# Performance work log

Measured on AMD Instinct MI355X. Metric: run time of the kernel, lower is better.

The kernel has to match this reference:

```python
import jax, jax.numpy as jnp
import numpy as np

DIM = 1024
HEADS = 16
HIDDEN = 2048  # dim * mlp_ratio
EPS = 1e-6


def _rmsnorm(x, scale):
    # faithful to torch: x * (scale / (norm / (sqrt(d) + eps)))
    norm = jnp.linalg.norm(x, axis=-1, keepdims=True)
    return x * (scale * (x.shape[-1] ** 0.5 + EPS) / norm)


def setup_inputs() -> dict:
    key = jax.random.key(0)
    ks = jax.random.split(key, 8)
    B, N, C = 4, 4096, DIM
    s = 0.02
    return {
        "x": jax.random.normal(ks[0], (B, N, C), dtype=jnp.float32),
        "scale1": jnp.ones((C,), jnp.float32),
        "scale2": jnp.ones((C,), jnp.float32),
        "gamma": jnp.ones((C,), jnp.float32),
        "qkv_w": jax.random.normal(ks[1], (3 * C, C), jnp.float32) * s,
        "proj_w": jax.random.normal(ks[2], (C, C), jnp.float32) * s,
        "proj_b": jnp.zeros((C,), jnp.float32),
        "conv1_w": jax.random.normal(ks[3], (HIDDEN, C), jnp.float32) * s,
        "conv1_b": jnp.zeros((HIDDEN,), jnp.float32),
        "conv2_w": jax.random.normal(ks[4], (C, HIDDEN), jnp.float32) * s,
        "conv2_b": jnp.zeros((C,), jnp.float32),
    }


def reference(x, scale1, scale2, gamma, qkv_w, proj_w, proj_b,
              conv1_w, conv1_b, conv2_w, conv2_b):
    B, N, C = x.shape
    h, d = HEADS, C // HEADS

    # ---- attention branch ----
    xn = _rmsnorm(x, scale1)
    qkv = jnp.einsum('bnc,fc->bnf', xn, qkv_w)           # [B,N,3C]
    qkv = qkv.reshape(B, N, 3, h, d).transpose(2, 0, 3, 1, 4)  # [3,B,h,N,d]
    q, k, v = qkv[0], qkv[1], qkv[2]
    phi = lambda t: jnp.exp(-0.5 * t * t)
    q, k = phi(q), phi(k)
    kv = jnp.einsum('bhnd,bhne->bhde', k, v)             # [B,h,d,d]
    z = 1.0 / (jnp.einsum('bhnd,bhd->bhn', q, k.sum(2)) + 1e-6)
    out = jnp.einsum('bhnd,bhde,bhn->bhne', q, kv, z)    # [B,h,N,d]
    out = out.transpose(0, 2, 1, 3).reshape(B, N, C)
    attn = jnp.einsum('bnc,oc->bno', out, proj_w) + proj_b
    x = x + gamma * attn

    # ---- MLP branch (1x1 convs == per-token linear) ----
    xn2 = _rmsnorm(x, scale2)
    hdd = jax.nn.gelu(jnp.einsum('bnc,hc->bnh', xn2, conv1_w) + conv1_b, approximate=False)
    mlp = jnp.einsum('bnh,ch->bnc', hdd, conv2_w) + conv2_b
    return x + gamma * mlp
```

## Files before the change

kernel.cpp:

```cpp
#include <hip/hip_runtime.h>
#include <hip/hip_bf16.h>
#include <math.h>

#define MTOK 16384

typedef __attribute__((ext_vector_type(8))) short bf16x8;
typedef __attribute__((ext_vector_type(4))) float f32x4;

__device__ __forceinline__ float bf2f(ushort u) {
  union { unsigned int u; float f; } c; c.u = ((unsigned int)u) << 16; return c.f;
}
__device__ __forceinline__ ushort f2bf(float f) {
  union { float f; unsigned int u; } c; c.f = f;
  unsigned int r = c.u + 0x7fffu + ((c.u >> 16) & 1u);
  return (ushort)(r >> 16);
}

__device__ __forceinline__ void gload_lds16(const void* g, void* l) {
  __builtin_amdgcn_global_load_lds(
      (const __attribute__((address_space(1))) unsigned int*)g,
      (__attribute__((address_space(3))) unsigned int*)l, 16, 0, 0);
}

__global__ __launch_bounds__(256)
void f32_to_bf16_k(const float* __restrict__ in, ushort* __restrict__ out, int n4) {
  int i = blockIdx.x * 256 + threadIdx.x;
  if (i >= n4) return;
  float4 v = *(const float4*)&in[(size_t)i * 4];
  ushort4 o;
  o.x = f2bf(v.x); o.y = f2bf(v.y); o.z = f2bf(v.z); o.w = f2bf(v.w);
  *(ushort4*)&out[(size_t)i * 4] = o;
}

__global__ __launch_bounds__(256)
void f32_to_bf16_rs_k(const float* __restrict__ in, ushort* __restrict__ out,
                      int n4, const float* __restrict__ rs, int K_in) {
  int i = blockIdx.x * 256 + threadIdx.x;
  if (i >= n4) return;
  float g = rs[(i * 4) / K_in];
  float4 v = *(const float4*)&in[(size_t)i * 4];
  ushort4 o;
  o.x = f2bf(v.x * g); o.y = f2bf(v.y * g); o.z = f2bf(v.z * g); o.w = f2bf(v.w * g);
  *(ushort4*)&out[(size_t)i * 4] = o;
}

__global__ __launch_bounds__(256)
void gbias_k(const float* __restrict__ gamma, const float* __restrict__ bias,
             float* __restrict__ gb, int n) {
  int i = blockIdx.x * 256 + threadIdx.x;
  if (i < n) gb[i] = gamma[i] * bias[i];
}

__global__ __launch_bounds__(256)
void rmsnorm_k(const float* __restrict__ x, const float* __restrict__ scale,
               ushort* __restrict__ out) {
  __shared__ float red[4];
  int row = blockIdx.x;
  int t = threadIdx.x;
  const float* xr = x + (size_t)row * 1024;
  float4 v = *(const float4*)&xr[t * 4];
  float s = v.x*v.x + v.y*v.y + v.z*v.z + v.w*v.w;
  #pragma unroll
  for (int off = 32; off > 0; off >>= 1) s += __shfl_xor(s, off);
  if ((t & 63) == 0) red[t >> 6] = s;
  __syncthreads();
  float tot = red[0] + red[1] + red[2] + red[3];
  float rn = (32.0f + 1e-6f) / sqrtf(tot);
  float4 sc = *(const float4*)&scale[t * 4];
  ushort4 o;
  o.x = f2bf(v.x * rn * sc.x);
  o.y = f2bf(v.y * rn * sc.y);
  o.z = f2bf(v.z * rn * sc.z);
  o.w = f2bf(v.w * rn * sc.w);
  *(ushort4*)&out[(size_t)row * 1024 + t * 4] = o;
}

template<int EPI>
__global__ __launch_bounds__(256, 2)
void gemm_bt(const ushort* __restrict__ A, const ushort* __restrict__ W,
             void* __restrict__ outp, const float* __restrict__ bias,
             const float* __restrict__ resid,
             ushort* __restrict__ kTp, ushort* __restrict__ vTp,
             int M, int F, int K) {
  __shared__ ushort lA[2][128 * 32];
  __shared__ ushort lB[2][128 * 32];
  const int tid = threadIdx.x;
  const int lane = tid & 63;
  const int w = tid >> 6;
  const int nBn = F >> 7;
  const int cpx = (int)gridDim.x >> 3;
  const int tile = ((int)blockIdx.x & 7) * cpx + ((int)blockIdx.x >> 3);
  const int bm = tile / nBn;
  const int bn = tile % nBn;
  const int brow = bm << 7, bcol = bn << 7;
  const int wr = w >> 1, wc = w & 1;

  const int srow = (w << 4) + (lane >> 2);
  const int key = (srow >> 1) & 3;
  const int kcsrc = (lane & 3) ^ key;
  const ushort* gA0 = A + (size_t)(brow + srow) * K + kcsrc * 8;
  const ushort* gA1 = gA0 + (size_t)64 * K;
  const ushort* gB0 = W + (size_t)(bcol + srow) * K + kcsrc * 8;
  const ushort* gB1 = gB0 + (size_t)64 * K;

  auto stage = [&](int bf, int k0) {
    gload_lds16(gA0 + k0, &lA[bf][w * 512]);
    gload_lds16(gA1 + k0, &lA[bf][2048 + w * 512]);
    gload_lds16(gB0 + k0, &lB[bf][w * 512]);
    gload_lds16(gB1 + k0, &lB[bf][2048 + w * 512]);
  };

  const int frow = lane & 15;
  const int kq = lane >> 4;

  f32x4 acc[4][4];
  #pragma unroll
  for (int i = 0; i < 4; ++i)
    #pragma unroll
    for (int j = 0; j < 4; ++j) acc[i][j] = (f32x4){0.f, 0.f, 0.f, 0.f};

  stage(0, 0);
  __syncthreads();

  int buf = 0;
  for (int k0 = 0; k0 < K; k0 += 32, buf ^= 1) {
    if (k0 + 32 < K) stage(buf ^ 1, k0 + 32);

    bf16x8 af[4], bfr[4];
    #pragma unroll
    for (int mi = 0; mi < 4; ++mi) {
      int row = (wr << 6) + (mi << 4) + frow;
      int off = (row << 5) + ((kq ^ ((row >> 1) & 3)) << 3);
      af[mi] = *(const bf16x8*)&lA[buf][off];
    }
    #pragma unroll
    for (int ni = 0; ni < 4; ++ni) {
      int row = (wc << 6) + (ni << 4) + frow;
      int off = (row << 5) + ((kq ^ ((row >> 1) & 3)) << 3);
      bfr[ni] = *(const bf16x8*)&lB[buf][off];
    }
    #pragma unroll
    for (int mi = 0; mi < 4; ++mi)
      #pragma unroll
      for (int ni = 0; ni < 4; ++ni)
        acc[mi][ni] = __builtin_amdgcn_mfma_f32_16x16x32_bf16(
            af[mi], bfr[ni], acc[mi][ni], 0, 0, 0);
    __syncthreads();
  }

  #pragma unroll
  for (int mi = 0; mi < 4; ++mi) {
    #pragma unroll
    for (int ni = 0; ni < 4; ++ni) {
      int col = bcol + (wc << 6) + (ni << 4) + frow;
      int rbase = brow + (wr << 6) + (mi << 4) + (kq << 2);
      if (EPI == 0) {
        if (col < 1024) {
          #pragma unroll
          for (int r = 0; r < 4; ++r) {
            float v = acc[mi][ni][r];
            ((ushort*)outp)[(size_t)(rbase + r) * 1024 + col] =
                f2bf(__expf(-0.5f * v * v));
          }
        } else {
          bool isk = col < 2048;
          int c = col - (isk ? 1024 : 2048);
          int b = rbase >> 12, n = rbase & 4095;
          ushort4 o;
          #pragma unroll
          for (int r = 0; r < 4; ++r) {
            float v = acc[mi][ni][r];
            if (isk) v = __expf(-0.5f * v * v);
            ((ushort*)&o)[r] = f2bf(v);
          }
          ushort* dst = (isk ? kTp : vTp) +
                        ((size_t)(b * 16 + (c >> 6)) * 64 + (c & 63)) * 4096 + n;
          *(ushort4*)dst = o;
        }
      } else {
        #pragma unroll
        for (int r = 0; r < 4; ++r) {
          int row = rbase + r;
          float v = acc[mi][ni][r];
          size_t idx = (size_t)row * F + col;
          if (EPI == 1) {
            ((float*)outp)[idx] = resid[idx] + v + bias[col];
          } else {
            float t2 = v + bias[col];
            float y = 0.79788456f * (t2 + 0.044715f * t2 * t2 * t2);
            float e = __expf(2.0f * y);
            float th = (e - 1.0f) / (e + 1.0f);
            ((ushort*)outp)[idx] = f2bf(0.5f * t2 * (1.0f + th));
          }
        }
      }
    }
  }
}

__global__ __launch_bounds__(256)
void attn_kv_mfma(const ushort* __restrict__ kT, const ushort* __restrict__ vT,
                  float* __restrict__ kvT, float* __restrict__ ksum) {
  __shared__ float red[4][4096];
  int bi = blockIdx.x;
  int ksl = bi & 7, h = (bi >> 3) & 15, b = bi >> 7;
  int tid = threadIdx.x, lane = tid & 63, w = tid >> 6;
  int frow = lane & 15, kq = lane >> 4;
  const size_t bh = (size_t)(b * 16 + h) * 64;
  const ushort* vb = vT + bh * 4096;
  const ushort* kb = kT + bh * 4096;
  int tk0 = ksl * 512 + w * 128;

  f32x4 acc[4][4];
  #pragma unroll
  for (int i = 0; i < 4; ++i)
    #pragma unroll
    for (int j = 0; j < 4; ++j) acc[i][j] = (f32x4){0.f, 0.f, 0.f, 0.f};
  float kpart[4] = {0.f, 0.f, 0.f, 0.f};

  #pragma unroll
  for (int kstep = 0; kstep < 4; ++kstep) {
    int tok = tk0 + kstep * 32 + kq * 8;
    bf16x8 af[4], bfr[4];
    #pragma unroll
    for (int mi = 0; mi < 4; ++mi)
      af[mi] = *(const bf16x8*)&vb[(size_t)(mi * 16 + frow) * 4096 + tok];
    #pragma unroll
    for (int ni = 0; ni < 4; ++ni) {
      bfr[ni] = *(const bf16x8*)&kb[(size_t)(ni * 16 + frow) * 4096 + tok];
      #pragma unroll
      for (int j = 0; j < 8; ++j) kpart[ni] += bf2f((ushort)bfr[ni][j]);
    }
    #pragma unroll
    for (int mi = 0; mi < 4; ++mi)
      #pragma unroll
      for (int ni = 0; ni < 4; ++ni)
        acc[mi][ni] = __builtin_amdgcn_mfma_f32_16x16x32_bf16(
            af[mi], bfr[ni], acc[mi][ni], 0, 0, 0);
  }

  #pragma unroll
  for (int ni = 0; ni < 4; ++ni) {
    kpart[ni] += __shfl_xor(kpart[ni], 16);
    kpart[ni] += __shfl_xor(kpart[ni], 32);
  }
  if (lane < 16) {
    #pragma unroll
    for (int ni = 0; ni < 4; ++ni)
      atomicAdd(&ksum[(b * 16 + h) * 64 + ni * 16 + frow], kpart[ni]);
  }

  #pragma unroll
  for (int mi = 0; mi < 4; ++mi)
    #pragma unroll
    for (int ni = 0; ni < 4; ++ni)
      #pragma unroll
      for (int r = 0; r < 4; ++r)
        red[w][(mi * 16 + kq * 4 + r) * 64 + ni * 16 + frow] = acc[mi][ni][r];
  __syncthreads();
  float* kvg = kvT + (size_t)(b * 16 + h) * 4096;
  for (int i = tid; i < 4096; i += 256) {
    float s = red[0][i] + red[1][i] + red[2][i] + red[3][i];
    atomicAdd(&kvg[i], s);
  }
}

__global__ __launch_bounds__(256)
void attn_out_mfma(const ushort* __restrict__ qb, const float* __restrict__ kvT,
                   const float* __restrict__ ksum, ushort* __restrict__ ao) {
  __shared__ ushort skv[64 * 72];
  __shared__ float sks[64];
  int bi = blockIdx.x;
  int c = bi & 15, h = (bi >> 4) & 15, b = bi >> 8;
  int tid = threadIdx.x, lane = tid & 63, w = tid >> 6;
  int frow = lane & 15, kq = lane >> 4;
  const float* kvg = kvT + (size_t)(b * 16 + h) * 4096;
  for (int i = tid; i < 4096; i += 256)
    skv[(i >> 6) * 72 + (i & 63)] = f2bf(kvg[i]);
  if (tid < 64) sks[tid] = ksum[(b * 16 + h) * 64 + tid];
  __syncthreads();

  int m0 = b * 4096 + c * 256 + w * 64;
  f32x4 acc[4][4];
  #pragma unroll
  for (int i = 0; i < 4; ++i)
    #pragma unroll
    for (int j = 0; j < 4; ++j) acc[i][j] = (f32x4){0.f, 0.f, 0.f, 0.f};
  float dp[4] = {0.f, 0.f, 0.f, 0.f};

  #pragma unroll
  for (int kst = 0; kst < 2; ++kst) {
    int d0 = kst * 32 + kq * 8;
    bf16x8 af[4], bfr[4];
    #pragma unroll
    for (int mi = 0; mi < 4; ++mi)
      af[mi] = *(const bf16x8*)&qb[(size_t)(m0 + mi * 16 + frow) * 1024 + h * 64 + d0];
    #pragma unroll
    for (int ni = 0; ni < 4; ++ni)
      bfr[ni] = *(const bf16x8*)&skv[(ni * 16 + frow) * 72 + d0];
    #pragma unroll
    for (int mi = 0; mi < 4; ++mi) {
      float s = 0.f;
      #pragma unroll
      for (int j = 0; j < 8; ++j) s += bf2f((ushort)af[mi][j]) * sks[d0 + j];
      dp[mi] += s;
    }
    #pragma unroll
    for (int mi = 0; mi < 4; ++mi)
      #pragma unroll
      for (int ni = 0; ni < 4; ++ni)
        acc[mi][ni] = __builtin_amdgcn_mfma_f32_16x16x32_bf16(
            af[mi], bfr[ni], acc[mi][ni], 0, 0, 0);
  }

  #pragma unroll
  for (int mi = 0; mi < 4; ++mi) {
    dp[mi] += __shfl_xor(dp[mi], 16);
    dp[mi] += __shfl_xor(dp[mi], 32);
  }

  #pragma unroll
  for (int mi = 0; mi < 4; ++mi)
    #pragma unroll
    for (int ni = 0; ni < 4; ++ni)
      #pragma unroll
      for (int r = 0; r < 4; ++r) {
        float dotv = __shfl(dp[mi], (kq << 2) + r);
        float z = 1.f / (dotv + 1e-6f);
        int mrow = m0 + mi * 16 + kq * 4 + r;
        ao[(size_t)mrow * 1024 + h * 64 + ni * 16 + frow] =
            f2bf(acc[mi][ni][r] * z);
      }
}

extern "C" void kernel_launch(void* const* d_in, const int* in_sizes, int n_in,
                              void* d_out, int out_size, void* d_ws, size_t ws_size,
                              hipStream_t stream) {
  const float* x       = (const float*)d_in[0];
  const float* scale1  = (const float*)d_in[1];
  const float* scale2  = (const float*)d_in[2];
  const float* gamma   = (const float*)d_in[3];
  const float* qkv_w   = (const float*)d_in[4];
  const float* proj_w  = (const float*)d_in[5];
  const float* proj_b  = (const float*)d_in[6];
  const float* conv1_w = (const float*)d_in[7];
  const float* conv1_b = (const float*)d_in[8];
  const float* conv2_w = (const float*)d_in[9];
  const float* conv2_b = (const float*)d_in[10];
  float* out = (float*)d_out;

  char* ws = (char*)d_ws;
  size_t off = 0;
  auto alloc = [&](size_t bytes) {
    void* p = ws + off;
    off += (bytes + 255) & ~(size_t)255;
    return p;
  };
  ushort* xn     = (ushort*)alloc((size_t)MTOK * 1024 * 2);
  ushort* qb     = (ushort*)alloc((size_t)MTOK * 1024 * 2);
  ushort* kT     = (ushort*)alloc((size_t)MTOK * 1024 * 2);
  ushort* vT     = (ushort*)alloc((size_t)MTOK * 1024 * 2);
  ushort* attn_o = (ushort*)alloc((size_t)MTOK * 1024 * 2);
  float*  kvT    = (float*)alloc((size_t)(4 * 16 * 64 * 64 + 4 * 16 * 64) * 4);
  float*  ksum   = kvT + 4 * 16 * 64 * 64;
  ushort* wq = (ushort*)alloc((size_t)3072 * 1024 * 2);
  ushort* wp = (ushort*)alloc((size_t)1024 * 1024 * 2);
  ushort* w1 = (ushort*)alloc((size_t)2048 * 1024 * 2);
  ushort* w2 = (ushort*)alloc((size_t)1024 * 2048 * 2);
  float*  gbp = (float*)alloc(1024 * 4);
  float*  gbc = (float*)alloc(1024 * 4);
  ushort* hid = kT;
  if (off > ws_size) return;

  hipMemsetAsync(kvT, 0, (size_t)(4 * 16 * 64 * 64 + 4 * 16 * 64) * 4, stream);
  f32_to_bf16_k<<<3072, 256, 0, stream>>>(qkv_w, wq, 786432);
  f32_to_bf16_rs_k<<<1024, 256, 0, stream>>>(proj_w, wp, 262144, gamma, 1024);
  f32_to_bf16_k<<<2048, 256, 0, stream>>>(conv1_w, w1, 524288);
  f32_to_bf16_rs_k<<<2048, 256, 0, stream>>>(conv2_w, w2, 524288, gamma, 2048);
  gbias_k<<<4, 256, 0, stream>>>(gamma, proj_b, gbp, 1024);
  gbias_k<<<4, 256, 0, stream>>>(gamma, conv2_b, gbc, 1024);

  rmsnorm_k<<<MTOK, 256, 0, stream>>>(x, scale1, xn);
  gemm_bt<0><<<128 * 24, 256, 0, stream>>>(xn, wq, qb, nullptr, nullptr,
                                           kT, vT, MTOK, 3072, 1024);
  attn_kv_mfma<<<512, 256, 0, stream>>>(kT, vT, kvT, ksum);
  attn_out_mfma<<<1024, 256, 0, stream>>>(qb, kvT, ksum, attn_o);
  gemm_bt<1><<<128 * 8, 256, 0, stream>>>(attn_o, wp, out, gbp, x,
                                          nullptr, nullptr, MTOK, 1024, 1024);

  rmsnorm_k<<<MTOK, 256, 0, stream>>>(out, scale2, xn);
  gemm_bt<2><<<128 * 16, 256, 0, stream>>>(xn, w1, hid, conv1_b, nullptr,
                                           nullptr, nullptr, MTOK, 2048, 1024);
  gemm_bt<1><<<128 * 8, 256, 0, stream>>>(hid, w2, out, gbc, out,
                                          nullptr, nullptr, MTOK, 1024, 2048);
}
```

Baseline: 463.4 us.

## Switch GEMM to 32x32 MFMA and fuse second RMSNorm into proj epilogue

The GEMM inner loop now uses 32x32x16 bf16 MFMA with 2x2 fragments per wave instead of 4x4 16x16x32 fragments, and every epilogue is rewritten for the new accumulator layout. The proj GEMM gets a new epilogue that writes the residual output, emits unnormalized scale2-weighted bf16 activations, and accumulates per-row sum of squares through LDS and global atomics. A small kernel turns those sums into reciprocal norms, which the conv1 GEMM epilogue applies per row. This removes the separate rmsnorm pass over the fp32 residual, at the cost of atomics, heavier epilogue traffic, and a bf16 rounding of the pre-normalized value.

After: 524.6 us. 1.13x slower.

```diff
diff --git a/kernel.cpp b/kernel.cpp
--- a/kernel.cpp
+++ b/kernel.cpp
@@ -6,6 +6,7 @@
 
 typedef __attribute__((ext_vector_type(8))) short bf16x8;
 typedef __attribute__((ext_vector_type(4))) float f32x4;
+typedef __attribute__((ext_vector_type(16))) float f32x16;
 
 __device__ __forceinline__ float bf2f(ushort u) {
   union { unsigned int u; float f; } c; c.u = ((unsigned int)u) << 16; return c.f;
@@ -49,6 +50,12 @@
              float* __restrict__ gb, int n) {
   int i = blockIdx.x * 256 + threadIdx.x;
   if (i < n) gb[i] = gamma[i] * bias[i];
+}
+
+__global__ __launch_bounds__(256)
+void rn_k(const float* __restrict__ sumsq, float* __restrict__ rn, int n) {
+  int i = blockIdx.x * 256 + threadIdx.x;
+  if (i < n) rn[i] = (32.0f + 1e-6f) / sqrtf(sumsq[i]);
 }
 
 __global__ __launch_bounds__(256)
@@ -81,6 +88,8 @@
              void* __restrict__ outp, const float* __restrict__ bias,
              const float* __restrict__ resid,
              ushort* __restrict__ kTp, ushort* __restrict__ vTp,
+             const float* __restrict__ escale, const float* __restrict__ rowscale,
+             float* __restrict__ sumsq, ushort* __restrict__ xnout,
              int M, int F, int K) {
   __shared__ ushort lA[2][128 * 32];
   __shared__ ushort lB[2][128 * 32];
@@ -110,14 +119,16 @@
     gload_lds16(gB1 + k0, &lB[bf][2048 + w * 512]);
   };
 
-  const int frow = lane & 15;
-  const int kq = lane >> 4;
-
-  f32x4 acc[4][4];
-  #pragma unroll
-  for (int i = 0; i < 4; ++i)
-    #pragma unroll
-    for (int j = 0; j < 4; ++j) acc[i][j] = (f32x4){0.f, 0.f, 0.f, 0.f};
+  const int l31 = lane & 31;
+  const int lh = lane >> 5;
+
+  f32x16 acc16[2][2];
+  #pragma unroll
+  for (int i = 0; i < 2; ++i)
+    #pragma unroll
+    for (int j = 0; j < 2; ++j)
+      #pragma unroll
+      for (int r = 0; r < 16; ++r) acc16[i][j][r] = 0.f;
 
   stage(0, 0);
   __syncthreads();
@@ -126,75 +137,111 @@
   for (int k0 = 0; k0 < K; k0 += 32, buf ^= 1) {
     if (k0 + 32 < K) stage(buf ^ 1, k0 + 32);
 
-    bf16x8 af[4], bfr[4];
-    #pragma unroll
-    for (int mi = 0; mi < 4; ++mi) {
-      int row = (wr << 6) + (mi << 4) + frow;
-      int off = (row << 5) + ((kq ^ ((row >> 1) & 3)) << 3);
-      af[mi] = *(const bf16x8*)&lA[buf][off];
+    #pragma unroll
+    for (int kh = 0; kh < 2; ++kh) {
+      bf16x8 ar[2], br[2];
+      #pragma unroll
+      for (int mi = 0; mi < 2; ++mi) {
+        int row = (wr << 6) + (mi << 5) + l31;
+        int slot = (kh * 2 + lh) ^ ((row >> 1) & 3);
+        ar[mi] = *(const bf16x8*)&lA[buf][(row << 5) + (slot << 3)];
+      }
+      #pragma unroll
+      for (int ni = 0; ni < 2; ++ni) {
+        int row = (wc << 6) + (ni << 5) + l31;
+        int slot = (kh * 2 + lh) ^ ((row >> 1) & 3);
+        br[ni] = *(const bf16x8*)&lB[buf][(row << 5) + (slot << 3)];
+      }
+      #pragma unroll
+      for (int mi = 0; mi < 2; ++mi)
+        #pragma unroll
+        for (int ni = 0; ni < 2; ++ni)
+          acc16[mi][ni] = __builtin_amdgcn_mfma_f32_32x32x16_bf16(
+              ar[mi], br[ni], acc16[mi][ni], 0, 0, 0);
     }
-    #pragma unroll
-    for (int ni = 0; ni < 4; ++ni) {
-      int row = (wc << 6) + (ni << 4) + frow;
-      int off = (row << 5) + ((kq ^ ((row >> 1) & 3)) << 3);
-      bfr[ni] = *(const bf16x8*)&lB[buf][off];
-    }
-    #pragma unroll
-    for (int mi = 0; mi < 4; ++mi)
-      #pragma unroll
-      for (int ni = 0; ni < 4; ++ni)
-        acc[mi][ni] = __builtin_amdgcn_mfma_f32_16x16x32_bf16(
-            af[mi], bfr[ni], acc[mi][ni], 0, 0, 0);
     __syncthreads();
   }
 
-  #pragma unroll
-  for (int mi = 0; mi < 4; ++mi) {
-    #pragma unroll
-    for (int ni = 0; ni < 4; ++ni) {
-      int col = bcol + (wc << 6) + (ni << 4) + frow;
-      int rbase = brow + (wr << 6) + (mi << 4) + (kq << 2);
+  float* ldsS = (float*)&lA[0][0];
+  if (EPI == 3) {
+    if (tid < 128) ldsS[tid] = 0.f;
+    __syncthreads();
+  }
+
+  #pragma unroll
+  for (int mi = 0; mi < 2; ++mi) {
+    const int rb0 = brow + (wr << 6) + (mi << 5) + (lh << 2);
+    #pragma unroll
+    for (int ni = 0; ni < 2; ++ni) {
+      const int col = bcol + (wc << 6) + (ni << 5) + l31;
       if (EPI == 0) {
         if (col < 1024) {
           #pragma unroll
-          for (int r = 0; r < 4; ++r) {
-            float v = acc[mi][ni][r];
-            ((ushort*)outp)[(size_t)(rbase + r) * 1024 + col] =
+          for (int reg = 0; reg < 16; ++reg) {
+            int row = rb0 + (reg & 3) + ((reg >> 2) << 3);
+            float v = acc16[mi][ni][reg];
+            ((ushort*)outp)[(size_t)row * 1024 + col] =
                 f2bf(__expf(-0.5f * v * v));
           }
         } else {
           bool isk = col < 2048;
           int c = col - (isk ? 1024 : 2048);
-          int b = rbase >> 12, n = rbase & 4095;
-          ushort4 o;
+          ushort* base = (isk ? kTp : vTp) +
+                         ((size_t)((rb0 >> 12) * 16 + (c >> 6)) * 64 + (c & 63)) * 4096;
           #pragma unroll
-          for (int r = 0; r < 4; ++r) {
-            float v = acc[mi][ni][r];
-            if (isk) v = __expf(-0.5f * v * v);
-            ((ushort*)&o)[r] = f2bf(v);
+          for (int q2 = 0; q2 < 4; ++q2) {
+            int n0 = rb0 + (q2 << 3);
+            ushort4 o;
+            #pragma unroll
+            for (int j = 0; j < 4; ++j) {
+              float v = acc16[mi][ni][q2 * 4 + j];
+              if (isk) v = __expf(-0.5f * v * v);
+              ((ushort*)&o)[j] = f2bf(v);
+            }
+            *(ushort4*)&base[n0 & 4095] = o;
           }
-          ushort* dst = (isk ? kTp : vTp) +
-                        ((size_t)(b * 16 + (c >> 6)) * 64 + (c & 63)) * 4096 + n;
-          *(ushort4*)dst = o;
         }
-      } else {
+      } else if (EPI == 1) {
         #pragma unroll
-        for (int r = 0; r < 4; ++r) {
-          int row = rbase + r;
-          float v = acc[mi][ni][r];
+        for (int reg = 0; reg < 16; ++reg) {
+          int row = rb0 + (reg & 3) + ((reg >> 2) << 3);
           size_t idx = (size_t)row * F + col;
-          if (EPI == 1) {
-            ((float*)outp)[idx] = resid[idx] + v + bias[col];
-          } else {
-            float t2 = v + bias[col];
-            float y = 0.79788456f * (t2 + 0.044715f * t2 * t2 * t2);
-            float e = __expf(2.0f * y);
-            float th = (e - 1.0f) / (e + 1.0f);
-            ((ushort*)outp)[idx] = f2bf(0.5f * t2 * (1.0f + th));
-          }
+          ((float*)outp)[idx] = resid[idx] + acc16[mi][ni][reg] + bias[col];
+        }
+      } else if (EPI == 2) {
+        #pragma unroll
+        for (int reg = 0; reg < 16; ++reg) {
+          int row = rb0 + (reg & 3) + ((reg >> 2) << 3);
+          float t2 = acc16[mi][ni][reg] * rowscale[row] + bias[col];
+          float y = 0.79788456f * (t2 + 0.044715f * t2 * t2 * t2);
+          float e = __expf(2.0f * y);
+          float th = (e - 1.0f) / (e + 1.0f);
+          ((ushort*)outp)[(size_t)row * F + col] = f2bf(0.5f * t2 * (1.0f + th));
         }
       }
     }
+    if (EPI == 3) {
+      #pragma unroll
+      for (int reg = 0; reg < 16; ++reg) {
+        int row = rb0 + (reg & 3) + ((reg >> 2) << 3);
+        float ss = 0.f;
+        #pragma unroll
+        for (int ni = 0; ni < 2; ++ni) {
+          int col = bcol + (wc << 6) + (ni << 5) + l31;
+          size_t idx = (size_t)row * F + col;
+          float x1 = resid[idx] + acc16[mi][ni][reg] + bias[col];
+          ((float*)outp)[idx] = x1;
+          xnout[idx] = f2bf(x1 * escale[col]);
+          ss += x1 * x1;
+        }
+        atomicAdd(&ldsS[row - brow], ss);
+      }
+    }
+  }
+
+  if (EPI == 3) {
+    __syncthreads();
+    if (tid < 128) atomicAdd(&sumsq[brow + tid], ldsS[tid]);
   }
 }
 
@@ -369,10 +416,13 @@
   ushort* w2 = (ushort*)alloc((size_t)1024 * 2048 * 2);
   float*  gbp = (float*)alloc(1024 * 4);
   float*  gbc = (float*)alloc(1024 * 4);
+  float*  sumsq = (float*)alloc(MTOK * 4);
+  float*  rnb   = (float*)alloc(MTOK * 4);
   ushort* hid = kT;
   if (off > ws_size) return;
 
   hipMemsetAsync(kvT, 0, (size_t)(4 * 16 * 64 * 64 + 4 * 16 * 64) * 4, stream);
+  hipMemsetAsync(sumsq, 0, MTOK * 4, stream);
   f32_to_bf16_k<<<3072, 256, 0, stream>>>(qkv_w, wq, 786432);
   f32_to_bf16_rs_k<<<1024, 256, 0, stream>>>(proj_w, wp, 262144, gamma, 1024);
   f32_to_bf16_k<<<2048, 256, 0, stream>>>(conv1_w, w1, 524288);
@@ -382,15 +432,19 @@
 
   rmsnorm_k<<<MTOK, 256, 0, stream>>>(x, scale1, xn);
   gemm_bt<0><<<128 * 24, 256, 0, stream>>>(xn, wq, qb, nullptr, nullptr,
-                                           kT, vT, MTOK, 3072, 1024);
+                                           kT, vT, nullptr, nullptr, nullptr, nullptr,
+                                           MTOK, 3072, 1024);
   attn_kv_mfma<<<512, 256, 0, stream>>>(kT, vT, kvT, ksum);
   attn_out_mfma<<<1024, 256, 0, stream>>>(qb, kvT, ksum, attn_o);
-  gemm_bt<1><<<128 * 8, 256, 0, stream>>>(attn_o, wp, out, gbp, x,
-                                          nullptr, nullptr, MTOK, 1024, 1024);
-
-  rmsnorm_k<<<MTOK, 256, 0, stream>>>(out, scale2, xn);
+  gemm_bt<3><<<128 * 8, 256, 0, stream>>>(attn_o, wp, out, gbp, x,
+                                          nullptr, nullptr, scale2, nullptr,
+                                          sumsq, xn, MTOK, 1024, 1024);
+  rn_k<<<64, 256, 0, stream>>>(sumsq, rnb, MTOK);
+
   gemm_bt<2><<<128 * 16, 256, 0, stream>>>(xn, w1, hid, conv1_b, nullptr,
+                                           nullptr, nullptr, nullptr, rnb,
                                            nullptr, nullptr, MTOK, 2048, 1024);
   gemm_bt<1><<<128 * 8, 256, 0, stream>>>(hid, w2, out, gbc, out,
+                                          nullptr, nullptr, nullptr, nullptr,
                                           nullptr, nullptr, MTOK, 1024, 2048);
 }
```

## Fuse second RMSNorm into proj GEMM epilogue with deferred row scaling

Applied to the files above, without the earlier changes.

The attention projection GEMM epilogue now writes the residual sum, emits an unnormalized bf16 copy scaled by scale2, and accumulates per-row sum of squares through LDS and global atomics. A tiny kernel converts those sums to reciprocal norms, and the conv1 GEMM applies the row scale to its accumulator before bias and GELU. This removes a full-activation rmsnorm pass that re-read the fp32 residual stream. In exchange it adds atomics, an extra memset and launch, and feeds unnormalized bf16 values into the GEMM, which can change rounding error.

After: 472.2 us. About the same (+1.9%).

```diff
diff --git a/kernel.cpp b/kernel.cpp
--- a/kernel.cpp
+++ b/kernel.cpp
@@ -49,6 +49,12 @@
              float* __restrict__ gb, int n) {
   int i = blockIdx.x * 256 + threadIdx.x;
   if (i < n) gb[i] = gamma[i] * bias[i];
+}
+
+__global__ __launch_bounds__(256)
+void rn_k(const float* __restrict__ sumsq, float* __restrict__ rn, int n) {
+  int i = blockIdx.x * 256 + threadIdx.x;
+  if (i < n) rn[i] = (32.0f + 1e-6f) / sqrtf(sumsq[i]);
 }
 
 __global__ __launch_bounds__(256)
@@ -81,6 +87,8 @@
              void* __restrict__ outp, const float* __restrict__ bias,
              const float* __restrict__ resid,
              ushort* __restrict__ kTp, ushort* __restrict__ vTp,
+             const float* __restrict__ escale, const float* __restrict__ rowscale,
+             float* __restrict__ sumsq, ushort* __restrict__ xnout,
              int M, int F, int K) {
   __shared__ ushort lA[2][128 * 32];
   __shared__ ushort lB[2][128 * 32];
@@ -148,12 +156,19 @@
     __syncthreads();
   }
 
+  float* ldsS = (float*)&lA[0][0];
+  if (EPI == 3) {
+    if (tid < 128) ldsS[tid] = 0.f;
+    __syncthreads();
+  }
+
   #pragma unroll
   for (int mi = 0; mi < 4; ++mi) {
+    const int rbase = brow + (wr << 6) + (mi << 4) + (kq << 2);
+    float ss[4] = {0.f, 0.f, 0.f, 0.f};
     #pragma unroll
     for (int ni = 0; ni < 4; ++ni) {
       int col = bcol + (wc << 6) + (ni << 4) + frow;
-      int rbase = brow + (wr << 6) + (mi << 4) + (kq << 2);
       if (EPI == 0) {
         if (col < 1024) {
           #pragma unroll
@@ -177,24 +192,43 @@
                         ((size_t)(b * 16 + (c >> 6)) * 64 + (c & 63)) * 4096 + n;
           *(ushort4*)dst = o;
         }
+      } else if (EPI == 1) {
+        #pragma unroll
+        for (int r = 0; r < 4; ++r) {
+          size_t idx = (size_t)(rbase + r) * F + col;
+          ((float*)outp)[idx] = resid[idx] + acc[mi][ni][r] + bias[col];
+        }
+      } else if (EPI == 2) {
+        #pragma unroll
+        for (int r = 0; r < 4; ++r) {
+          float t2 = acc[mi][ni][r] * rowscale[rbase + r] + bias[col];
+          float y = 0.79788456f * (t2 + 0.044715f * t2 * t2 * t2);
+          float e = __expf(2.0f * y);
+          float th = (e - 1.0f) / (e + 1.0f);
+          ((ushort*)outp)[(size_t)(rbase + r) * F + col] =
+              f2bf(0.5f * t2 * (1.0f + th));
+        }
       } else {
         #pragma unroll
         for (int r = 0; r < 4; ++r) {
-          int row = rbase + r;
-          float v = acc[mi][ni][r];
-          size_t idx = (size_t)row * F + col;
-          if (EPI == 1) {
-            ((float*)outp)[idx] = resid[idx] + v + bias[col];
-          } else {
-            float t2 = v + bias[col];
-            float y = 0.79788456f * (t2 + 0.044715f * t2 * t2 * t2);
-            float e = __expf(2.0f * y);
-            float th = (e - 1.0f) / (e + 1.0f);
-            ((ushort*)outp)[idx] = f2bf(0.5f * t2 * (1.0f + th));
-          }
+          size_t idx = (size_t)(rbase + r) * F + col;
+          float x1 = resid[idx] + acc[mi][ni][r] + bias[col];
+          ((float*)outp)[idx] = x1;
+          xnout[idx] = f2bf(x1 * escale[col]);
+          ss[r] += x1 * x1;
         }
       }
     }
+    if (EPI == 3) {
+      #pragma unroll
+      for (int r = 0; r < 4; ++r)
+        atomicAdd(&ldsS[rbase - brow + r], ss[r]);
+    }
+  }
+
+  if (EPI == 3) {
+    __syncthreads();
+    if (tid < 128) atomicAdd(&sumsq[brow + tid], ldsS[tid]);
   }
 }
 
@@ -369,10 +403,13 @@
   ushort* w2 = (ushort*)alloc((size_t)1024 * 2048 * 2);
   float*  gbp = (float*)alloc(1024 * 4);
   float*  gbc = (float*)alloc(1024 * 4);
+  float*  sumsq = (float*)alloc(MTOK * 4);
+  float*  rnb   = (float*)alloc(MTOK * 4);
   ushort* hid = kT;
   if (off > ws_size) return;
 
   hipMemsetAsync(kvT, 0, (size_t)(4 * 16 * 64 * 64 + 4 * 16 * 64) * 4, stream);
+  hipMemsetAsync(sumsq, 0, MTOK * 4, stream);
   f32_to_bf16_k<<<3072, 256, 0, stream>>>(qkv_w, wq, 786432);
   f32_to_bf16_rs_k<<<1024, 256, 0, stream>>>(proj_w, wp, 262144, gamma, 1024);
   f32_to_bf16_k<<<2048, 256, 0, stream>>>(conv1_w, w1, 524288);
@@ -382,15 +419,19 @@
 
   rmsnorm_k<<<MTOK, 256, 0, stream>>>(x, scale1, xn);
   gemm_bt<0><<<128 * 24, 256, 0, stream>>>(xn, wq, qb, nullptr, nullptr,
-                                           kT, vT, MTOK, 3072, 1024);
+                                           kT, vT, nullptr, nullptr, nullptr, nullptr,
+                                           MTOK, 3072, 1024);
   attn_kv_mfma<<<512, 256, 0, stream>>>(kT, vT, kvT, ksum);
   attn_out_mfma<<<1024, 256, 0, stream>>>(qb, kvT, ksum, attn_o);
-  gemm_bt<1><<<128 * 8, 256, 0, stream>>>(attn_o, wp, out, gbp, x,
-                                          nullptr, nullptr, MTOK, 1024, 1024);
-
-  rmsnorm_k<<<MTOK, 256, 0, stream>>>(out, scale2, xn);
+  gemm_bt<3><<<128 * 8, 256, 0, stream>>>(attn_o, wp, out, gbp, x,
+                                          nullptr, nullptr, scale2, nullptr,
+                                          sumsq, xn, MTOK, 1024, 1024);
+  rn_k<<<64, 256, 0, stream>>>(sumsq, rnb, MTOK);
+
   gemm_bt<2><<<128 * 16, 256, 0, stream>>>(xn, w1, hid, conv1_b, nullptr,
+                                           nullptr, nullptr, nullptr, rnb,
                                            nullptr, nullptr, MTOK, 2048, 1024);
   gemm_bt<1><<<128 * 8, 256, 0, stream>>>(hid, w2, out, gbc, out,
+                                          nullptr, nullptr, nullptr, nullptr,
                                           nullptr, nullptr, MTOK, 1024, 2048);
 }
```
